# Kernel optimization log

Measured on AMD Instinct MI355X. Metric: run time of the kernel, lower is better.

## Reference

```python
import jax, jax.numpy as jnp
import numpy as np
import math

L, N, D = 1024, 64, 64
O = 1024

def setup_inputs() -> dict:
    key = jax.random.key(0)
    k1, k2 = jax.random.split(key)
    x = jax.random.normal(k1, (L, N, D), dtype=jnp.float32)
    upfold = jax.random.normal(k2, (O, N, D), dtype=jnp.float32)
    return {"x": x, "upfold": upfold}

def reference(x, upfold):
    # x: [L, N, D], upfold: [O, N, D]
    d = x.shape[-1]
    scale = 1.0 / math.sqrt(d)
    # affinities: [L, O, N]
    affinities = jnp.einsum('lnd,ond->lon', x, upfold) * scale
    # weighted sum with (sigmoid - 0.5) weights: [L, N, D]
    features = jnp.einsum('lon,ond->lnd', jax.nn.sigmoid(affinities) - 0.5, upfold)
    return features
```

## Files before the change

kernel.cpp:

```cpp
#include <hip/hip_runtime.h>
#include <stdint.h>

#define L_DIM 1024
#define N_DIM 64
#define D_DIM 64
#define O_DIM 1024
#define ND    4096
#define NT    8

typedef float    floatx16 __attribute__((ext_vector_type(16)));
typedef _Float16 half8    __attribute__((ext_vector_type(8)));
typedef _Float16 h2       __attribute__((ext_vector_type(2)));
typedef __fp16   fp16x2   __attribute__((ext_vector_type(2)));

#define IMG_BYTES 16384
#define WS_NEEDED ((size_t)N_DIM * 16 * IMG_BYTES)

#define BUF_STRIDE_FB 17920

__device__ __forceinline__ uint32_t pkh2(float a, float b) {
    fp16x2 p = __builtin_amdgcn_cvt_pkrtz(a, b);
    return __builtin_bit_cast(uint32_t, p);
}

__device__ __forceinline__ half8 mk_frag(uint32_t a, uint32_t b, uint32_t c, uint32_t d) {
    union { uint32_t u[4]; half8 v; } U;
    U.u[0] = a; U.u[1] = b; U.u[2] = c; U.u[3] = d;
    return U.v;
}

__device__ __forceinline__ uint32_t psig(float s0, float s1) {
    const h2 HI = {(_Float16)41.6f,        (_Float16)41.6f};
    const h2 LO = {(_Float16)-41.6f,       (_Float16)-41.6f};
    const h2 SC = {(_Float16)0.0625f,      (_Float16)0.0625f};
    const h2 C0 = {(_Float16)0.03099238f,  (_Float16)0.03099238f};
    const h2 C1 = {(_Float16)-0.00842090f, (_Float16)-0.00842090f};
    const h2 C2 = {(_Float16)0.00151845f,  (_Float16)0.00151845f};
    const h2 C3 = {(_Float16)-1.02197e-4f, (_Float16)-1.02197e-4f};
    h2 s = __builtin_bit_cast(h2, pkh2(s0, s1));
    s = __builtin_elementwise_min(s, HI);
    s = __builtin_elementwise_max(s, LO);
    h2 ha = s * SC;
    h2 v  = ha * ha;
    h2 w  = C2 + v * C3;
    w     = C1 + v * w;
    w     = C0 + v * w;
    h2 f  = s * w;
    return __builtin_bit_cast(uint32_t, f);
}

__device__ __forceinline__ void load_tile(const float* ubase, int ot,
                                          int r8, int c, float4* va, float4* vb) {
    const float* pr = ubase + (size_t)(ot * 64 + 2 * r8) * ND + 4 * c;
    #pragma unroll
    for (int j = 0; j < 2; ++j) {
        va[j] = *(const float4*)(pr + (size_t)(32 * j) * ND);
        vb[j] = *(const float4*)(pr + (size_t)(32 * j) * ND + ND);
    }
}

__global__ void __launch_bounds__(256)
conv_kernel(const float* __restrict__ up, unsigned char* __restrict__ img)
{
    const int tid = threadIdx.x;
    const int r8  = tid >> 4;
    const int c   = tid & 15;
    const int n   = blockIdx.x;
    const int ot  = blockIdx.y;

    const float* ubase = up + (size_t)n * D_DIM;
    float4 va[2], vb[2];
    load_tile(ubase, ot, r8, c, va, vb);

    unsigned char* tb = img + (size_t)(n * 16 + ot) * IMG_BYTES;

    const int kk = c >> 2;
    const int hh = (c >> 1) & 1;
    const int co = (c & 1) * 8;
    #pragma unroll
    for (int j = 0; j < 2; ++j) {
        const int o0 = 2 * r8 + 32 * j;
        unsigned char* g1 = tb + j * 4096 + kk * 1024 + co;
        *(uint2*)(g1 + ((o0 & 31) + 32 * hh) * 16) =
            make_uint2(pkh2(va[j].x, va[j].y), pkh2(va[j].z, va[j].w));
        *(uint2*)(g1 + (((o0 + 1) & 31) + 32 * hh) * 16) =
            make_uint2(pkh2(vb[j].x, vb[j].y), pkh2(vb[j].z, vb[j].w));
    }

    #pragma unroll
    for (int j = 0; j < 2; ++j) {
        const int op   = r8 + 16 * j;
        const int g    = op >> 2;
        const int slot = op & 3;
        const int t2   = g >> 2;
        const int c22  = (g >> 1) & 1;
        const int h2i  = g & 1;
        const float* pa = (const float*)&va[j];
        const float* pb = (const float*)&vb[j];
        #pragma unroll
        for (int col = 0; col < 4; ++col) {
            const int d    = 4 * c + col;
            const int r    = d >> 5;
            const int lane = (d & 31) + 32 * h2i;
            *(uint32_t*)(tb + 8192 + t2 * 4096 + c22 * 2048 + r * 1024
                         + lane * 16 + slot * 4) = pkh2(pa[col], pb[col]);
        }
    }
}

__device__ __forceinline__ void load_frags(const unsigned char* tb, int team, int lane,
                                           half8* Ak, half8* G2) {
    const unsigned char* g1 = tb + team * 4096 + (size_t)lane * 16;
    #pragma unroll
    for (int kk = 0; kk < 4; ++kk)
        Ak[kk] = *(const half8*)(g1 + kk * 1024);
    const unsigned char* g2 = tb + 8192 + team * 4096 + (size_t)lane * 16;
    #pragma unroll
    for (int i = 0; i < 4; ++i)
        G2[i] = *(const half8*)(g2 + i * 1024);
}

__device__ __forceinline__ void compute_tile(const half8* Ak, const half8* G2,
                                             const half8* Xf0, const half8* Xf1, int h,
                                             floatx16& F00, floatx16& F01,
                                             floatx16& F10, floatx16& F11)
{
    floatx16 S0, S1;
    #pragma unroll
    for (int i = 0; i < 16; ++i) { S0[i] = 0.0f; S1[i] = 0.0f; }
    #pragma unroll
    for (int kk = 0; kk < 4; ++kk) {
        S0 = __builtin_amdgcn_mfma_f32_32x32x16_f16(Ak[kk], Xf0[kk], S0, 0, 0, 0);
        S1 = __builtin_amdgcn_mfma_f32_32x32x16_f16(Ak[kk], Xf1[kk], S1, 0, 0, 0);
    }

    uint32_t P0[8], P1[8];
    #pragma unroll
    for (int m = 0; m < 8; ++m) { P0[m] = psig(S0[2*m], S0[2*m+1]);
                                  P1[m] = psig(S1[2*m], S1[2*m+1]); }

    uint32_t R0[4], R1[4];
    #pragma unroll
    for (int c2 = 0; c2 < 2; ++c2) {
        const int t4 = c2 * 4;
        R0[2*c2]   = __shfl_xor(h ? P0[t4]     : P0[t4 + 2], 32);
        R0[2*c2+1] = __shfl_xor(h ? P0[t4 + 1] : P0[t4 + 3], 32);
        R1[2*c2]   = __shfl_xor(h ? P1[t4]     : P1[t4 + 2], 32);
        R1[2*c2+1] = __shfl_xor(h ? P1[t4 + 1] : P1[t4 + 3], 32);
    }
    #pragma unroll
    for (int c2 = 0; c2 < 2; ++c2) {
        const int t4 = c2 * 4;
        half8 B0 = h ? mk_frag(R0[2*c2], R0[2*c2+1], P0[t4 + 2], P0[t4 + 3])
                     : mk_frag(P0[t4], P0[t4 + 1], R0[2*c2], R0[2*c2+1]);
        half8 B1 = h ? mk_frag(R1[2*c2], R1[2*c2+1], P1[t4 + 2], P1[t4 + 3])
                     : mk_frag(P1[t4], P1[t4 + 1], R1[2*c2], R1[2*c2+1]);
        F00 = __builtin_amdgcn_mfma_f32_32x32x16_f16(G2[2*c2],     B0, F00, 0, 0, 0);
        F01 = __builtin_amdgcn_mfma_f32_32x32x16_f16(G2[2*c2 + 1], B0, F01, 0, 0, 0);
        F10 = __builtin_amdgcn_mfma_f32_32x32x16_f16(G2[2*c2],     B1, F10, 0, 0, 0);
        F11 = __builtin_amdgcn_mfma_f32_32x32x16_f16(G2[2*c2 + 1], B1, F11, 0, 0, 0);
    }
}

__global__ void __launch_bounds__(512, 2)
corr_kernel_w(const float* __restrict__ x, const unsigned char* __restrict__ img,
              float* __restrict__ out)
{
    __shared__ __align__(16) float Xs[256][68];

    const int tid  = threadIdx.x;
    const int lane = tid & 63;
    const int wid  = tid >> 6;
    const int team = wid >> 2;
    const int tw   = wid & 3;
    const int l31  = lane & 31;
    const int h    = lane >> 5;
    const int n    = blockIdx.x;
    const int lb   = blockIdx.y;

    const unsigned char* gimg = img + (size_t)n * 16 * IMG_BYTES;

    half8 Xf0[4], Xf1[4];
    {
        const int xr = tid >> 1;
        const int xh = tid & 1;
        const float* xsrc = x + (size_t)(lb * 256 + xr) * ND + n * D_DIM;
        #pragma unroll
        for (int j = 0; j < 8; ++j) {
            const int f4i = xh * 8 + j;
            *(float4*)&Xs[xr][4 * f4i] = *(const float4*)(xsrc + 4 * f4i);
        }
        __syncthreads();
        const int rl0 = tw * 64 + l31;
        const int rl1 = rl0 + 32;
        #pragma unroll
        for (int kk = 0; kk < 4; ++kk) {
            float4 f1 = *(const float4*)&Xs[rl0][16 * kk + 8 * h];
            float4 f2 = *(const float4*)&Xs[rl0][16 * kk + 8 * h + 4];
            Xf0[kk] = mk_frag(pkh2(f1.x, f1.y), pkh2(f1.z, f1.w),
                              pkh2(f2.x, f2.y), pkh2(f2.z, f2.w));
            float4 f3 = *(const float4*)&Xs[rl1][16 * kk + 8 * h];
            float4 f4v = *(const float4*)&Xs[rl1][16 * kk + 8 * h + 4];
            Xf1[kk] = mk_frag(pkh2(f3.x, f3.y), pkh2(f3.z, f3.w),
                              pkh2(f4v.x, f4v.y), pkh2(f4v.z, f4v.w));
        }
        __syncthreads();
    }

    floatx16 F00, F01, F10, F11;
    #pragma unroll
    for (int i = 0; i < 16; ++i) { F00[i] = 0.0f; F01[i] = 0.0f;
                                   F10[i] = 0.0f; F11[i] = 0.0f; }

    half8 AkE[4], G2E[4], AkO[4], G2O[4];
    load_frags(gimg, team, lane, AkE, G2E);
    for (int ot = 0; ot < 16; ot += 2) {
        load_frags(gimg + (size_t)(ot + 1) * IMG_BYTES, team, lane, AkO, G2O);
        compute_tile(AkE, G2E, Xf0, Xf1, h, F00, F01, F10, F11);
        if (ot + 2 < 16)
            load_frags(gimg + (size_t)(ot + 2) * IMG_BYTES, team, lane, AkE, G2E);
        compute_tile(AkO, G2O, Xf0, Xf1, h, F00, F01, F10, F11);
    }

    {
        if (team == 1) {
            #pragma unroll
            for (int lh = 0; lh < 2; ++lh) {
                const int row = tw * 64 + lh * 32 + l31;
                const floatx16& A = lh ? F10 : F00;
                const floatx16& Bq = lh ? F11 : F01;
                #pragma unroll
                for (int q = 0; q < 4; ++q) {
                    float4 a; a.x = A[4*q]; a.y = A[4*q+1]; a.z = A[4*q+2]; a.w = A[4*q+3];
                    *(float4*)&Xs[row][8*q + 4*h] = a;
                    float4 b2; b2.x = Bq[4*q]; b2.y = Bq[4*q+1]; b2.z = Bq[4*q+2]; b2.w = Bq[4*q+3];
                    *(float4*)&Xs[row][32 + 8*q + 4*h] = b2;
                }
            }
        }
        __syncthreads();
        if (team == 0) {
            #pragma unroll
            for (int lh = 0; lh < 2; ++lh) {
                const int row = tw * 64 + lh * 32 + l31;
                const floatx16& A = lh ? F10 : F00;
                const floatx16& Bq = lh ? F11 : F01;
                float* op = out + (size_t)(lb * 256 + row) * ND + n * D_DIM;
                #pragma unroll
                for (int q = 0; q < 4; ++q) {
                    float4 t0 = *(const float4*)&Xs[row][8*q + 4*h];
                    float4 a; a.x = A[4*q]   + t0.x; a.y = A[4*q+1] + t0.y;
                              a.z = A[4*q+2] + t0.z; a.w = A[4*q+3] + t0.w;
                    *(float4*)(op + 8*q + 4*h) = a;
                    float4 t1 = *(const float4*)&Xs[row][32 + 8*q + 4*h];
                    float4 b2; b2.x = Bq[4*q]   + t1.x; b2.y = Bq[4*q+1] + t1.y;
                               b2.z = Bq[4*q+2] + t1.z; b2.w = Bq[4*q+3] + t1.w;
                    *(float4*)(op + 32 + 8*q + 4*h) = b2;
                }
            }
        }
    }
}

__global__ void __launch_bounds__(512, 4)
corr_kernel_fb(const float* __restrict__ x, const float* __restrict__ up,
               float* __restrict__ out)
{
    __shared__ __align__(16) unsigned char smem[4 * BUF_STRIDE_FB];

    const int tid  = threadIdx.x;
    const int lane = tid & 63;
    const int wid  = tid >> 6;
    const int team = wid >> 2;
    const int tw   = wid & 3;
    const int l31  = lane & 31;
    const int h    = lane >> 5;
    const int ttid = tid & 255;
    const int r8   = ttid >> 4;
    const int c    = ttid & 15;
    const int n    = blockIdx.x;
    const int lb   = blockIdx.y;
    const int lw   = lb * 128 + tw * 32 + l31;

    const float* ubase = up + (size_t)n * D_DIM;
    const int ob = team * NT;
    unsigned char* tsmem = smem + team * 2 * BUF_STRIDE_FB;

    float4 va[2], vb[2];
    load_tile(ubase, ob + 0, r8, c, va, vb);

    half8 Xf[4];
    {
        float (*Xs)[68] = (float (*)[68])smem;
        const int xr = tid >> 2;
        const int xq = tid & 3;
        const float* xsrc = x + (size_t)(lb * 128 + xr) * ND + n * D_DIM;
        #pragma unroll
        for (int j = 0; j < 4; ++j) {
            const int f4i = xq * 4 + j;
            *(float4*)&Xs[xr][4 * f4i] = *(const float4*)(xsrc + 4 * f4i);
        }
        __syncthreads();
        const int rl = tw * 32 + l31;
        #pragma unroll
        for (int kk = 0; kk < 4; ++kk) {
            float4 f1 = *(const float4*)&Xs[rl][16 * kk + 8 * h];
            float4 f2 = *(const float4*)&Xs[rl][16 * kk + 8 * h + 4];
            Xf[kk] = mk_frag(pkh2(f1.x, f1.y), pkh2(f1.z, f1.w),
                             pkh2(f2.x, f2.y), pkh2(f2.z, f2.w));
        }
        __syncthreads();
    }

    #pragma unroll
    for (int j = 0; j < 2; ++j) {
        uint16_t (*Ub)[72]  = (uint16_t (*)[72])(tsmem);
        uint32_t (*Ut2)[68] = (uint32_t (*)[68])(tsmem + 9216);
        *(uint2*)&Ub[2*r8 + 32*j][4*c] =
            make_uint2(pkh2(va[j].x, va[j].y), pkh2(va[j].z, va[j].w));
        *(uint2*)&Ub[2*r8 + 32*j + 1][4*c] =
            make_uint2(pkh2(vb[j].x, vb[j].y), pkh2(vb[j].z, vb[j].w));
        *(uint4*)&Ut2[r8 + 16*j][4*c] =
            make_uint4(pkh2(va[j].x, vb[j].x), pkh2(va[j].y, vb[j].y),
                       pkh2(va[j].z, vb[j].z), pkh2(va[j].w, vb[j].w));
    }
    load_tile(ubase, ob + 1, r8, c, va, vb);
    __syncthreads();

    floatx16 F0, F1;
    #pragma unroll
    for (int i = 0; i < 16; ++i) { F0[i] = 0.0f; F1[i] = 0.0f; }

    for (int ot = 0; ot < NT; ++ot) {
        const int b = ot & 1;
        uint16_t (*Ub)[72]   = (uint16_t (*)[72])(tsmem + b * BUF_STRIDE_FB);
        const uint32_t* utp  = (const uint32_t*)(tsmem + b * BUF_STRIDE_FB + 9216);
        uint16_t (*Ubn)[72]  = (uint16_t (*)[72])(tsmem + (b ^ 1) * BUF_STRIDE_FB);
        uint32_t (*Ut2n)[68] = (uint32_t (*)[68])(tsmem + (b ^ 1) * BUF_STRIDE_FB + 9216);

        half8 A0k[4], A1k[4];
        #pragma unroll
        for (int kk = 0; kk < 4; ++kk) {
            A0k[kk] = *(const half8*)&Ub[l31][16 * kk + 8 * h];
            A1k[kk] = *(const half8*)&Ub[32 + l31][16 * kk + 8 * h];
        }

        if (ot + 1 < NT) {
            #pragma unroll
            for (int j = 0; j < 2; ++j) {
                *(uint2*)&Ubn[2*r8 + 32*j][4*c] =
                    make_uint2(pkh2(va[j].x, va[j].y), pkh2(va[j].z, va[j].w));
                *(uint2*)&Ubn[2*r8 + 32*j + 1][4*c] =
                    make_uint2(pkh2(vb[j].x, vb[j].y), pkh2(vb[j].z, vb[j].w));
                *(uint4*)&Ut2n[r8 + 16*j][4*c] =
                    make_uint4(pkh2(va[j].x, vb[j].x), pkh2(va[j].y, vb[j].y),
                               pkh2(va[j].z, vb[j].z), pkh2(va[j].w, vb[j].w));
            }
        }
        if (ot + 2 < NT)
            load_tile(ubase, ob + ot + 2, r8, c, va, vb);

        floatx16 S0, S1;
        #pragma unroll
        for (int i = 0; i < 16; ++i) { S0[i] = 0.0f; S1[i] = 0.0f; }
        #pragma unroll
        for (int kk = 0; kk < 4; ++kk) {
            S0 = __builtin_amdgcn_mfma_f32_32x32x16_f16(A0k[kk], Xf[kk], S0, 0, 0, 0);
            S1 = __builtin_amdgcn_mfma_f32_32x32x16_f16(A1k[kk], Xf[kk], S1, 0, 0, 0);
        }

        uint32_t P[16];
        #pragma unroll
        for (int m = 0; m < 8; ++m) P[m]     = psig(S0[2*m], S0[2*m+1]);
        #pragma unroll
        for (int m = 0; m < 8; ++m) P[8 + m] = psig(S1[2*m], S1[2*m+1]);

        uint32_t R[8];
        #pragma unroll
        for (int c2 = 0; c2 < 4; ++c2) {
            const uint32_t* Q = P + (c2 >> 1) * 8;
            const int t4 = (c2 & 1) * 4;
            R[2*c2]   = __shfl_xor(h ? Q[t4]     : Q[t4 + 2], 32);
            R[2*c2+1] = __shfl_xor(h ? Q[t4 + 1] : Q[t4 + 3], 32);
        }
        #pragma unroll
        for (int c2 = 0; c2 < 4; ++c2) {
            const uint32_t* Q = P + (c2 >> 1) * 8;
            const int t4 = (c2 & 1) * 4;
            half8 B = h ? mk_frag(R[2*c2], R[2*c2+1], Q[t4 + 2], Q[t4 + 3])
                        : mk_frag(Q[t4], Q[t4 + 1], R[2*c2], R[2*c2+1]);
            const int opb = 8 * c2 + 4 * h;
            uint32_t a0[4], a1[4];
            #pragma unroll
            for (int k = 0; k < 4; ++k) {
                a0[k] = utp[(opb + k) * 68 + l31];
                a1[k] = utp[(opb + k) * 68 + 32 + l31];
            }
            half8 A0 = mk_frag(a0[0], a0[1], a0[2], a0[3]);
            half8 A1 = mk_frag(a1[0], a1[1], a1[2], a1[3]);
            F0 = __builtin_amdgcn_mfma_f32_32x32x16_f16(A0, B, F0, 0, 0, 0);
            F1 = __builtin_amdgcn_mfma_f32_32x32x16_f16(A1, B, F1, 0, 0, 0);
        }
        __syncthreads();
    }

    {
        float (*Fs)[68] = (float (*)[68])smem;
        const int row = tw * 32 + l31;
        if (team == 1) {
            #pragma unroll
            for (int q = 0; q < 4; ++q) {
                float4 a; a.x = F0[4*q]; a.y = F0[4*q+1]; a.z = F0[4*q+2]; a.w = F0[4*q+3];
                *(float4*)&Fs[row][8*q + 4*h] = a;
                float4 bq; bq.x = F1[4*q]; bq.y = F1[4*q+1]; bq.z = F1[4*q+2]; bq.w = F1[4*q+3];
                *(float4*)&Fs[row][32 + 8*q + 4*h] = bq;
            }
        }
        __syncthreads();
        if (team == 0) {
            float* op = out + (size_t)lw * ND + n * D_DIM;
            #pragma unroll
            for (int q = 0; q < 4; ++q) {
                float4 t0 = *(const float4*)&Fs[row][8*q + 4*h];
                float4 a; a.x = F0[4*q]   + t0.x; a.y = F0[4*q+1] + t0.y;
                          a.z = F0[4*q+2] + t0.z; a.w = F0[4*q+3] + t0.w;
                *(float4*)(op + 8*q + 4*h) = a;
                float4 t1 = *(const float4*)&Fs[row][32 + 8*q + 4*h];
                float4 bq; bq.x = F1[4*q]   + t1.x; bq.y = F1[4*q+1] + t1.y;
                           bq.z = F1[4*q+2] + t1.z; bq.w = F1[4*q+3] + t1.w;
                *(float4*)(op + 32 + 8*q + 4*h) = bq;
            }
        }
    }
}

extern "C" void kernel_launch(void* const* d_in, const int* in_sizes, int n_in,
                              void* d_out, int out_size, void* d_ws, size_t ws_size,
                              hipStream_t stream)
{
    const float* x  = (const float*)d_in[0];
    const float* up = (const float*)d_in[1];
    float* out      = (float*)d_out;

    if (d_ws != nullptr && ws_size >= WS_NEEDED) {
        unsigned char* img = (unsigned char*)d_ws;
        conv_kernel<<<dim3(N_DIM, 16), dim3(256), 0, stream>>>(up, img);
        corr_kernel_w<<<dim3(N_DIM, L_DIM / 256), dim3(512), 0, stream>>>(x, img, out);
    } else {
        corr_kernel_fb<<<dim3(N_DIM, L_DIM / 128), dim3(512), 0, stream>>>(x, up, out);
    }
}
```

Baseline: 108.9 us.

## Fuse conversion and correlation kernels via cooperative launch with grid sync

Merges the upfold fp16 fragment-image conversion and the correlation kernel into one cooperative kernel. Each block first converts its share of the upfold tiles into the workspace, then a grid-wide barrier runs before the main MFMA computation. This aims to remove the second launch and the gap between the kernels. The cost is a grid sync, and 256 blocks of 512 threads must all be co-resident. If the cooperative launch fails, it falls back to the old two-kernel path.

```diff
diff --git a/kernel.cpp b/kernel.cpp
--- a/kernel.cpp
+++ b/kernel.cpp
@@ -1,4 +1,5 @@
 #include <hip/hip_runtime.h>
+#include <hip/hip_cooperative_groups.h>
 #include <stdint.h>
 
 #define L_DIM 1024
@@ -59,21 +60,9 @@
     }
 }
 
-__global__ void __launch_bounds__(256)
-conv_kernel(const float* __restrict__ up, unsigned char* __restrict__ img)
-{
-    const int tid = threadIdx.x;
-    const int r8  = tid >> 4;
-    const int c   = tid & 15;
-    const int n   = blockIdx.x;
-    const int ot  = blockIdx.y;
-
-    const float* ubase = up + (size_t)n * D_DIM;
-    float4 va[2], vb[2];
-    load_tile(ubase, ot, r8, c, va, vb);
-
-    unsigned char* tb = img + (size_t)(n * 16 + ot) * IMG_BYTES;
-
+__device__ __forceinline__ void pack_frag_image(unsigned char* tb, int r8, int c,
+                                                const float4* va, const float4* vb)
+{
     const int kk = c >> 2;
     const int hh = (c >> 1) & 1;
     const int co = (c & 1) * 8;
@@ -86,7 +75,6 @@
         *(uint2*)(g1 + (((o0 + 1) & 31) + 32 * hh) * 16) =
             make_uint2(pkh2(vb[j].x, vb[j].y), pkh2(vb[j].z, vb[j].w));
     }
-
     #pragma unroll
     for (int j = 0; j < 2; ++j) {
         const int op   = r8 + 16 * j;
@@ -106,6 +94,21 @@
                          + lane * 16 + slot * 4) = pkh2(pa[col], pb[col]);
         }
     }
+}
+
+__global__ void __launch_bounds__(256)
+conv_kernel(const float* __restrict__ up, unsigned char* __restrict__ img)
+{
+    const int tid = threadIdx.x;
+    const int r8  = tid >> 4;
+    const int c   = tid & 15;
+    const int n   = blockIdx.x;
+    const int ot  = blockIdx.y;
+
+    const float* ubase = up + (size_t)n * D_DIM;
+    float4 va[2], vb[2];
+    load_tile(ubase, ot, r8, c, va, vb);
+    pack_frag_image(img + (size_t)(n * 16 + ot) * IMG_BYTES, r8, c, va, vb);
 }
 
 __device__ __forceinline__ void load_frags(const unsigned char* tb, int team, int lane,
@@ -162,9 +165,96 @@
     }
 }
 
-__global__ void __launch_bounds__(512, 2)
-corr_kernel_w(const float* __restrict__ x, const unsigned char* __restrict__ img,
-              float* __restrict__ out)
+__device__ __forceinline__ void corr_body(const float* __restrict__ x,
+                                          const unsigned char* __restrict__ gimg,
+                                          float* __restrict__ out,
+                                          float (*Xs)[68],
+                                          int tid, int lane, int wid, int team,
+                                          int tw, int l31, int h, int n, int lb)
+{
+    half8 Xf0[4], Xf1[4];
+    {
+        const int xr = tid >> 1;
+        const int xh = tid & 1;
+        const float* xsrc = x + (size_t)(lb * 256 + xr) * ND + n * D_DIM;
+        #pragma unroll
+        for (int j = 0; j < 8; ++j) {
+            const int f4i = xh * 8 + j;
+            *(float4*)&Xs[xr][4 * f4i] = *(const float4*)(xsrc + 4 * f4i);
+        }
+        __syncthreads();
+        const int rl0 = tw * 64 + l31;
+        const int rl1 = rl0 + 32;
+        #pragma unroll
+        for (int kk = 0; kk < 4; ++kk) {
+            float4 f1 = *(const float4*)&Xs[rl0][16 * kk + 8 * h];
+            float4 f2 = *(const float4*)&Xs[rl0][16 * kk + 8 * h + 4];
+            Xf0[kk] = mk_frag(pkh2(f1.x, f1.y), pkh2(f1.z, f1.w),
+                              pkh2(f2.x, f2.y), pkh2(f2.z, f2.w));
+            float4 f3 = *(const float4*)&Xs[rl1][16 * kk + 8 * h];
+            float4 f4v = *(const float4*)&Xs[rl1][16 * kk + 8 * h + 4];
+            Xf1[kk] = mk_frag(pkh2(f3.x, f3.y), pkh2(f3.z, f3.w),
+                              pkh2(f4v.x, f4v.y), pkh2(f4v.z, f4v.w));
+        }
+        __syncthreads();
+    }
+
+    floatx16 F00, F01, F10, F11;
+    #pragma unroll
+    for (int i = 0; i < 16; ++i) { F00[i] = 0.0f; F01[i] = 0.0f;
+                                   F10[i] = 0.0f; F11[i] = 0.0f; }
+
+    half8 AkE[4], G2E[4], AkO[4], G2O[4];
+    load_frags(gimg, team, lane, AkE, G2E);
+    for (int ot = 0; ot < 16; ot += 2) {
+        load_frags(gimg + (size_t)(ot + 1) * IMG_BYTES, team, lane, AkO, G2O);
+        compute_tile(AkE, G2E, Xf0, Xf1, h, F00, F01, F10, F11);
+        if (ot + 2 < 16)
+            load_frags(gimg + (size_t)(ot + 2) * IMG_BYTES, team, lane, AkE, G2E);
+        compute_tile(AkO, G2O, Xf0, Xf1, h, F00, F01, F10, F11);
+    }
+
+    if (team == 1) {
+        #pragma unroll
+        for (int lh = 0; lh < 2; ++lh) {
+            const int row = tw * 64 + lh * 32 + l31;
+            const floatx16& A = lh ? F10 : F00;
+            const floatx16& Bq = lh ? F11 : F01;
+            #pragma unroll
+            for (int q = 0; q < 4; ++q) {
+                float4 a; a.x = A[4*q]; a.y = A[4*q+1]; a.z = A[4*q+2]; a.w = A[4*q+3];
+                *(float4*)&Xs[row][8*q + 4*h] = a;
+                float4 b2; b2.x = Bq[4*q]; b2.y = Bq[4*q+1]; b2.z = Bq[4*q+2]; b2.w = Bq[4*q+3];
+                *(float4*)&Xs[row][32 + 8*q + 4*h] = b2;
+            }
+        }
+    }
+    __syncthreads();
+    if (team == 0) {
+        #pragma unroll
+        for (int lh = 0; lh < 2; ++lh) {
+            const int row = tw * 64 + lh * 32 + l31;
+            const floatx16& A = lh ? F10 : F00;
+            const floatx16& Bq = lh ? F11 : F01;
+            float* op = out + (size_t)(lb * 256 + row) * ND + n * D_DIM;
+            #pragma unroll
+            for (int q = 0; q < 4; ++q) {
+                float4 t0 = *(const float4*)&Xs[row][8*q + 4*h];
+                float4 a; a.x = A[4*q]   + t0.x; a.y = A[4*q+1] + t0.y;
+                          a.z = A[4*q+2] + t0.z; a.w = A[4*q+3] + t0.w;
+                *(float4*)(op + 8*q + 4*h) = a;
+                float4 t1 = *(const float4*)&Xs[row][32 + 8*q + 4*h];
+                float4 b2; b2.x = Bq[4*q]   + t1.x; b2.y = Bq[4*q+1] + t1.y;
+                           b2.z = Bq[4*q+2] + t1.z; b2.w = Bq[4*q+3] + t1.w;
+                *(float4*)(op + 32 + 8*q + 4*h) = b2;
+            }
+        }
+    }
+}
+
+__global__ void __launch_bounds__(512, 1)
+corr_coop(const float* __restrict__ x, const float* __restrict__ up,
+          unsigned char* __restrict__ img, float* __restrict__ out)
 {
     __shared__ __align__(16) float Xs[256][68];
 
@@ -178,88 +268,43 @@
     const int n    = blockIdx.x;
     const int lb   = blockIdx.y;
 
-    const unsigned char* gimg = img + (size_t)n * 16 * IMG_BYTES;
-
-    half8 Xf0[4], Xf1[4];
     {
-        const int xr = tid >> 1;
-        const int xh = tid & 1;
-        const float* xsrc = x + (size_t)(lb * 256 + xr) * ND + n * D_DIM;
-        #pragma unroll
-        for (int j = 0; j < 8; ++j) {
-            const int f4i = xh * 8 + j;
-            *(float4*)&Xs[xr][4 * f4i] = *(const float4*)(xsrc + 4 * f4i);
-        }
-        __syncthreads();
-        const int rl0 = tw * 64 + l31;
-        const int rl1 = rl0 + 32;
-        #pragma unroll
-        for (int kk = 0; kk < 4; ++kk) {
-            float4 f1 = *(const float4*)&Xs[rl0][16 * kk + 8 * h];
-            float4 f2 = *(const float4*)&Xs[rl0][16 * kk + 8 * h + 4];
-            Xf0[kk] = mk_frag(pkh2(f1.x, f1.y), pkh2(f1.z, f1.w),
-                              pkh2(f2.x, f2.y), pkh2(f2.z, f2.w));
-            float4 f3 = *(const float4*)&Xs[rl1][16 * kk + 8 * h];
-            float4 f4v = *(const float4*)&Xs[rl1][16 * kk + 8 * h + 4];
-            Xf1[kk] = mk_frag(pkh2(f3.x, f3.y), pkh2(f3.z, f3.w),
-                              pkh2(f4v.x, f4v.y), pkh2(f4v.z, f4v.w));
-        }
-        __syncthreads();
-    }
-
-    floatx16 F00, F01, F10, F11;
-    #pragma unroll
-    for (int i = 0; i < 16; ++i) { F00[i] = 0.0f; F01[i] = 0.0f;
-                                   F10[i] = 0.0f; F11[i] = 0.0f; }
-
-    half8 AkE[4], G2E[4], AkO[4], G2O[4];
-    load_frags(gimg, team, lane, AkE, G2E);
-    for (int ot = 0; ot < 16; ot += 2) {
-        load_frags(gimg + (size_t)(ot + 1) * IMG_BYTES, team, lane, AkO, G2O);
-        compute_tile(AkE, G2E, Xf0, Xf1, h, F00, F01, F10, F11);
-        if (ot + 2 < 16)
-            load_frags(gimg + (size_t)(ot + 2) * IMG_BYTES, team, lane, AkE, G2E);
-        compute_tile(AkO, G2O, Xf0, Xf1, h, F00, F01, F10, F11);
-    }
-
-    {
-        if (team == 1) {
-            #pragma unroll
-            for (int lh = 0; lh < 2; ++lh) {
-                const int row = tw * 64 + lh * 32 + l31;
-                const floatx16& A = lh ? F10 : F00;
-                const floatx16& Bq = lh ? F11 : F01;
-                #pragma unroll
-                for (int q = 0; q < 4; ++q) {
-                    float4 a; a.x = A[4*q]; a.y = A[4*q+1]; a.z = A[4*q+2]; a.w = A[4*q+3];
-                    *(float4*)&Xs[row][8*q + 4*h] = a;
-                    float4 b2; b2.x = Bq[4*q]; b2.y = Bq[4*q+1]; b2.z = Bq[4*q+2]; b2.w = Bq[4*q+3];
-                    *(float4*)&Xs[row][32 + 8*q + 4*h] = b2;
-                }
-            }
-        }
-        __syncthreads();
-        if (team == 0) {
-            #pragma unroll
-            for (int lh = 0; lh < 2; ++lh) {
-                const int row = tw * 64 + lh * 32 + l31;
-                const floatx16& A = lh ? F10 : F00;
-                const floatx16& Bq = lh ? F11 : F01;
-                float* op = out + (size_t)(lb * 256 + row) * ND + n * D_DIM;
-                #pragma unroll
-                for (int q = 0; q < 4; ++q) {
-                    float4 t0 = *(const float4*)&Xs[row][8*q + 4*h];
-                    float4 a; a.x = A[4*q]   + t0.x; a.y = A[4*q+1] + t0.y;
-                              a.z = A[4*q+2] + t0.z; a.w = A[4*q+3] + t0.w;
-                    *(float4*)(op + 8*q + 4*h) = a;
-                    float4 t1 = *(const float4*)&Xs[row][32 + 8*q + 4*h];
-                    float4 b2; b2.x = Bq[4*q]   + t1.x; b2.y = Bq[4*q+1] + t1.y;
-                               b2.z = Bq[4*q+2] + t1.z; b2.w = Bq[4*q+3] + t1.w;
-                    *(float4*)(op + 32 + 8*q + 4*h) = b2;
-                }
-            }
-        }
-    }
+        const int ttid = tid & 255;
+        const int g    = tid >> 8;
+        const int r8   = ttid >> 4;
+        const int c    = ttid & 15;
+        const float* ubase = up + (size_t)n * D_DIM;
+        #pragma unroll
+        for (int rd = 0; rd < 2; ++rd) {
+            const int ot = lb * 4 + 2 * rd + g;
+            float4 va[2], vb[2];
+            load_tile(ubase, ot, r8, c, va, vb);
+            pack_frag_image(img + (size_t)(n * 16 + ot) * IMG_BYTES, r8, c, va, vb);
+        }
+    }
+    __threadfence();
+    cooperative_groups::this_grid().sync();
+
+    corr_body(x, img + (size_t)n * 16 * IMG_BYTES, out, Xs,
+              tid, lane, wid, team, tw, l31, h, n, lb);
+}
+
+__global__ void __launch_bounds__(512, 2)
+corr_kernel_w(const float* __restrict__ x, const unsigned char* __restrict__ img,
+              float* __restrict__ out)
+{
+    __shared__ __align__(16) float Xs[256][68];
+    const int tid  = threadIdx.x;
+    const int lane = tid & 63;
+    const int wid  = tid >> 6;
+    const int team = wid >> 2;
+    const int tw   = wid & 3;
+    const int l31  = lane & 31;
+    const int h    = lane >> 5;
+    const int n    = blockIdx.x;
+    const int lb   = blockIdx.y;
+    corr_body(x, img + (size_t)n * 16 * IMG_BYTES, out, Xs,
+              tid, lane, wid, team, tw, l31, h, n, lb);
 }
 
 __global__ void __launch_bounds__(512, 4)
@@ -444,8 +489,14 @@
 
     if (d_ws != nullptr && ws_size >= WS_NEEDED) {
         unsigned char* img = (unsigned char*)d_ws;
-        conv_kernel<<<dim3(N_DIM, 16), dim3(256), 0, stream>>>(up, img);
-        corr_kernel_w<<<dim3(N_DIM, L_DIM / 256), dim3(512), 0, stream>>>(x, img, out);
+        void* args[] = { (void*)&x, (void*)&up, (void*)&img, (void*)&out };
+        hipError_t e = hipLaunchCooperativeKernel(
+            reinterpret_cast<void*>(corr_coop),
+            dim3(N_DIM, L_DIM / 256), dim3(512), args, 0, stream);
+        if (e != hipSuccess) {
+            conv_kernel<<<dim3(N_DIM, 16), dim3(256), 0, stream>>>(up, img);
+            corr_kernel_w<<<dim3(N_DIM, L_DIM / 256), dim3(512), 0, stream>>>(x, img, out);
+        }
     } else {
         corr_kernel_fb<<<dim3(N_DIM, L_DIM / 128), dim3(512), 0, stream>>>(x, up, out);
     }
```

New measurement: 217.1 us. 1.99x slower.

## Fuse upfold fp16 image conversion into the correlation kernel

Applied to the files above, without the earlier changes.

Removes the separate conversion kernel launch. Each correlation block now converts the full upfold image for its head into workspace, then runs the same MFMA correlation body on it. The aim is to drop one kernel launch and the inter-kernel dependency gap. In exchange, each head's conversion is done redundantly by all four L-blocks, which write identical bytes to the same workspace. That multiplies global read and write traffic and lengthens each block's prologue.

```diff
diff --git a/kernel.cpp b/kernel.cpp
--- a/kernel.cpp
+++ b/kernel.cpp
@@ -59,21 +59,9 @@
     }
 }
 
-__global__ void __launch_bounds__(256)
-conv_kernel(const float* __restrict__ up, unsigned char* __restrict__ img)
-{
-    const int tid = threadIdx.x;
-    const int r8  = tid >> 4;
-    const int c   = tid & 15;
-    const int n   = blockIdx.x;
-    const int ot  = blockIdx.y;
-
-    const float* ubase = up + (size_t)n * D_DIM;
-    float4 va[2], vb[2];
-    load_tile(ubase, ot, r8, c, va, vb);
-
-    unsigned char* tb = img + (size_t)(n * 16 + ot) * IMG_BYTES;
-
+__device__ __forceinline__ void pack_frag_image(unsigned char* tb, int r8, int c,
+                                                const float4* va, const float4* vb)
+{
     const int kk = c >> 2;
     const int hh = (c >> 1) & 1;
     const int co = (c & 1) * 8;
@@ -86,7 +74,6 @@
         *(uint2*)(g1 + (((o0 + 1) & 31) + 32 * hh) * 16) =
             make_uint2(pkh2(vb[j].x, vb[j].y), pkh2(vb[j].z, vb[j].w));
     }
-
     #pragma unroll
     for (int j = 0; j < 2; ++j) {
         const int op   = r8 + 16 * j;
@@ -162,9 +149,96 @@
     }
 }
 
+__device__ __forceinline__ void corr_body(const float* __restrict__ x,
+                                          const unsigned char* __restrict__ gimg,
+                                          float* __restrict__ out,
+                                          float (*Xs)[68],
+                                          int tid, int lane, int wid, int team,
+                                          int tw, int l31, int h, int n, int lb)
+{
+    half8 Xf0[4], Xf1[4];
+    {
+        const int xr = tid >> 1;
+        const int xh = tid & 1;
+        const float* xsrc = x + (size_t)(lb * 256 + xr) * ND + n * D_DIM;
+        #pragma unroll
+        for (int j = 0; j < 8; ++j) {
+            const int f4i = xh * 8 + j;
+            *(float4*)&Xs[xr][4 * f4i] = *(const float4*)(xsrc + 4 * f4i);
+        }
+        __syncthreads();
+        const int rl0 = tw * 64 + l31;
+        const int rl1 = rl0 + 32;
+        #pragma unroll
+        for (int kk = 0; kk < 4; ++kk) {
+            float4 f1 = *(const float4*)&Xs[rl0][16 * kk + 8 * h];
+            float4 f2 = *(const float4*)&Xs[rl0][16 * kk + 8 * h + 4];
+            Xf0[kk] = mk_frag(pkh2(f1.x, f1.y), pkh2(f1.z, f1.w),
+                              pkh2(f2.x, f2.y), pkh2(f2.z, f2.w));
+            float4 f3 = *(const float4*)&Xs[rl1][16 * kk + 8 * h];
+            float4 f4v = *(const float4*)&Xs[rl1][16 * kk + 8 * h + 4];
+            Xf1[kk] = mk_frag(pkh2(f3.x, f3.y), pkh2(f3.z, f3.w),
+                              pkh2(f4v.x, f4v.y), pkh2(f4v.z, f4v.w));
+        }
+        __syncthreads();
+    }
+
+    floatx16 F00, F01, F10, F11;
+    #pragma unroll
+    for (int i = 0; i < 16; ++i) { F00[i] = 0.0f; F01[i] = 0.0f;
+                                   F10[i] = 0.0f; F11[i] = 0.0f; }
+
+    half8 AkE[4], G2E[4], AkO[4], G2O[4];
+    load_frags(gimg, team, lane, AkE, G2E);
+    for (int ot = 0; ot < 16; ot += 2) {
+        load_frags(gimg + (size_t)(ot + 1) * IMG_BYTES, team, lane, AkO, G2O);
+        compute_tile(AkE, G2E, Xf0, Xf1, h, F00, F01, F10, F11);
+        if (ot + 2 < 16)
+            load_frags(gimg + (size_t)(ot + 2) * IMG_BYTES, team, lane, AkE, G2E);
+        compute_tile(AkO, G2O, Xf0, Xf1, h, F00, F01, F10, F11);
+    }
+
+    if (team == 1) {
+        #pragma unroll
+        for (int lh = 0; lh < 2; ++lh) {
+            const int row = tw * 64 + lh * 32 + l31;
+            const floatx16& A = lh ? F10 : F00;
+            const floatx16& Bq = lh ? F11 : F01;
+            #pragma unroll
+            for (int q = 0; q < 4; ++q) {
+                float4 a; a.x = A[4*q]; a.y = A[4*q+1]; a.z = A[4*q+2]; a.w = A[4*q+3];
+                *(float4*)&Xs[row][8*q + 4*h] = a;
+                float4 b2; b2.x = Bq[4*q]; b2.y = Bq[4*q+1]; b2.z = Bq[4*q+2]; b2.w = Bq[4*q+3];
+                *(float4*)&Xs[row][32 + 8*q + 4*h] = b2;
+            }
+        }
+    }
+    __syncthreads();
+    if (team == 0) {
+        #pragma unroll
+        for (int lh = 0; lh < 2; ++lh) {
+            const int row = tw * 64 + lh * 32 + l31;
+            const floatx16& A = lh ? F10 : F00;
+            const floatx16& Bq = lh ? F11 : F01;
+            float* op = out + (size_t)(lb * 256 + row) * ND + n * D_DIM;
+            #pragma unroll
+            for (int q = 0; q < 4; ++q) {
+                float4 t0 = *(const float4*)&Xs[row][8*q + 4*h];
+                float4 a; a.x = A[4*q]   + t0.x; a.y = A[4*q+1] + t0.y;
+                          a.z = A[4*q+2] + t0.z; a.w = A[4*q+3] + t0.w;
+                *(float4*)(op + 8*q + 4*h) = a;
+                float4 t1 = *(const float4*)&Xs[row][32 + 8*q + 4*h];
+                float4 b2; b2.x = Bq[4*q]   + t1.x; b2.y = Bq[4*q+1] + t1.y;
+                           b2.z = Bq[4*q+2] + t1.z; b2.w = Bq[4*q+3] + t1.w;
+                *(float4*)(op + 32 + 8*q + 4*h) = b2;
+            }
+        }
+    }
+}
+
 __global__ void __launch_bounds__(512, 2)
-corr_kernel_w(const float* __restrict__ x, const unsigned char* __restrict__ img,
-              float* __restrict__ out)
+corr_single(const float* __restrict__ x, const float* __restrict__ up,
+            unsigned char* img, float* __restrict__ out)
 {
     __shared__ __align__(16) float Xs[256][68];
 
@@ -178,88 +252,24 @@
     const int n    = blockIdx.x;
     const int lb   = blockIdx.y;
 
-    const unsigned char* gimg = img + (size_t)n * 16 * IMG_BYTES;
-
-    half8 Xf0[4], Xf1[4];
     {
-        const int xr = tid >> 1;
-        const int xh = tid & 1;
-        const float* xsrc = x + (size_t)(lb * 256 + xr) * ND + n * D_DIM;
-        #pragma unroll
-        for (int j = 0; j < 8; ++j) {
-            const int f4i = xh * 8 + j;
-            *(float4*)&Xs[xr][4 * f4i] = *(const float4*)(xsrc + 4 * f4i);
-        }
-        __syncthreads();
-        const int rl0 = tw * 64 + l31;
-        const int rl1 = rl0 + 32;
-        #pragma unroll
-        for (int kk = 0; kk < 4; ++kk) {
-            float4 f1 = *(const float4*)&Xs[rl0][16 * kk + 8 * h];
-            float4 f2 = *(const float4*)&Xs[rl0][16 * kk + 8 * h + 4];
-            Xf0[kk] = mk_frag(pkh2(f1.x, f1.y), pkh2(f1.z, f1.w),
-                              pkh2(f2.x, f2.y), pkh2(f2.z, f2.w));
-            float4 f3 = *(const float4*)&Xs[rl1][16 * kk + 8 * h];
-            float4 f4v = *(const float4*)&Xs[rl1][16 * kk + 8 * h + 4];
-            Xf1[kk] = mk_frag(pkh2(f3.x, f3.y), pkh2(f3.z, f3.w),
-                              pkh2(f4v.x, f4v.y), pkh2(f4v.z, f4v.w));
-        }
-        __syncthreads();
-    }
-
-    floatx16 F00, F01, F10, F11;
-    #pragma unroll
-    for (int i = 0; i < 16; ++i) { F00[i] = 0.0f; F01[i] = 0.0f;
-                                   F10[i] = 0.0f; F11[i] = 0.0f; }
-
-    half8 AkE[4], G2E[4], AkO[4], G2O[4];
-    load_frags(gimg, team, lane, AkE, G2E);
-    for (int ot = 0; ot < 16; ot += 2) {
-        load_frags(gimg + (size_t)(ot + 1) * IMG_BYTES, team, lane, AkO, G2O);
-        compute_tile(AkE, G2E, Xf0, Xf1, h, F00, F01, F10, F11);
-        if (ot + 2 < 16)
-            load_frags(gimg + (size_t)(ot + 2) * IMG_BYTES, team, lane, AkE, G2E);
-        compute_tile(AkO, G2O, Xf0, Xf1, h, F00, F01, F10, F11);
-    }
-
-    {
-        if (team == 1) {
-            #pragma unroll
-            for (int lh = 0; lh < 2; ++lh) {
-                const int row = tw * 64 + lh * 32 + l31;
-                const floatx16& A = lh ? F10 : F00;
-                const floatx16& Bq = lh ? F11 : F01;
-                #pragma unroll
-                for (int q = 0; q < 4; ++q) {
-                    float4 a; a.x = A[4*q]; a.y = A[4*q+1]; a.z = A[4*q+2]; a.w = A[4*q+3];
-                    *(float4*)&Xs[row][8*q + 4*h] = a;
-                    float4 b2; b2.x = Bq[4*q]; b2.y = Bq[4*q+1]; b2.z = Bq[4*q+2]; b2.w = Bq[4*q+3];
-                    *(float4*)&Xs[row][32 + 8*q + 4*h] = b2;
-                }
-            }
-        }
-        __syncthreads();
-        if (team == 0) {
-            #pragma unroll
-            for (int lh = 0; lh < 2; ++lh) {
-                const int row = tw * 64 + lh * 32 + l31;
-                const floatx16& A = lh ? F10 : F00;
-                const floatx16& Bq = lh ? F11 : F01;
-                float* op = out + (size_t)(lb * 256 + row) * ND + n * D_DIM;
-                #pragma unroll
-                for (int q = 0; q < 4; ++q) {
-                    float4 t0 = *(const float4*)&Xs[row][8*q + 4*h];
-                    float4 a; a.x = A[4*q]   + t0.x; a.y = A[4*q+1] + t0.y;
-                              a.z = A[4*q+2] + t0.z; a.w = A[4*q+3] + t0.w;
-                    *(float4*)(op + 8*q + 4*h) = a;
-                    float4 t1 = *(const float4*)&Xs[row][32 + 8*q + 4*h];
-                    float4 b2; b2.x = Bq[4*q]   + t1.x; b2.y = Bq[4*q+1] + t1.y;
-                               b2.z = Bq[4*q+2] + t1.z; b2.w = Bq[4*q+3] + t1.w;
-                    *(float4*)(op + 32 + 8*q + 4*h) = b2;
-                }
-            }
-        }
-    }
+        const int ttid = tid & 255;
+        const int g    = tid >> 8;
+        const int r8   = ttid >> 4;
+        const int c    = ttid & 15;
+        const float* ubase = up + (size_t)n * D_DIM;
+        unsigned char* nimg = img + (size_t)n * 16 * IMG_BYTES;
+        #pragma unroll 2
+        for (int rd = 0; rd < 8; ++rd) {
+            const int ot = 2 * rd + g;
+            float4 va[2], vb[2];
+            load_tile(ubase, ot, r8, c, va, vb);
+            pack_frag_image(nimg + (size_t)ot * IMG_BYTES, r8, c, va, vb);
+        }
+    }
+
+    corr_body(x, img + (size_t)n * 16 * IMG_BYTES, out, Xs,
+              tid, lane, wid, team, tw, l31, h, n, lb);
 }
 
 __global__ void __launch_bounds__(512, 4)
@@ -444,8 +454,7 @@
 
     if (d_ws != nullptr && ws_size >= WS_NEEDED) {
         unsigned char* img = (unsigned char*)d_ws;
-        conv_kernel<<<dim3(N_DIM, 16), dim3(256), 0, stream>>>(up, img);
-        corr_kernel_w<<<dim3(N_DIM, L_DIM / 256), dim3(512), 0, stream>>>(x, img, out);
+        corr_single<<<dim3(N_DIM, L_DIM / 256), dim3(512), 0, stream>>>(x, up, img, out);
     } else {
         corr_kernel_fb<<<dim3(N_DIM, L_DIM / 128), dim3(512), 0, stream>>>(x, up, out);
     }
```

New measurement: 119.6 us. 1.1x slower.
